# Kernel tuning notes

Measured on AMD Instinct MI355X. Metric: run time of the kernel, lower is better.

Reference implementation:

```python
import jax, jax.numpy as jnp
import numpy as np

N_HEAD = 16
CHUNK_SIZE = 64
TOP_B = 8
LOCAL_WINDOW = 256


def _l2_normalize(x, eps=1e-12):
    # matches torch F.normalize(dim=-1): x / max(||x||, eps)
    n = jnp.sqrt(jnp.sum(x * x, axis=-1, keepdims=True))
    return x / jnp.maximum(n, eps)


def setup_inputs() -> dict:
    key = jax.random.key(0)
    ks = jax.random.split(key, 9)
    B, T, C = 2, 2048, 1024
    s = lambda fan_in: 1.0 / np.sqrt(fan_in)
    return {
        "x": jax.random.normal(ks[0], (B, T, C), jnp.float32),
        "Wqkv": jax.random.normal(ks[1], (C, 3 * C), jnp.float32) * s(C),
        "bqkv": jax.random.normal(ks[2], (3 * C,), jnp.float32) * 0.02,
        "Wproj": jax.random.normal(ks[3], (C, C), jnp.float32) * s(C),
        "bproj": jax.random.normal(ks[4], (C,), jnp.float32) * 0.02,
        "Wrouter": jax.random.normal(ks[5], (C, 32), jnp.float32) * s(C),
        "brouter": jax.random.normal(ks[6], (32,), jnp.float32) * 0.02,
        "Wq_rt": jax.random.normal(ks[7], (C, 32), jnp.float32) * s(C),
        "bq_rt": jax.random.normal(ks[8], (32,), jnp.float32) * 0.02,
    }


def reference(x, Wqkv, bqkv, Wproj, bproj, Wrouter, brouter, Wq_rt, bq_rt):
    B, T, C = x.shape
    H = N_HEAD
    D = C // H

    # --- qkv projection ---
    qkv = x @ Wqkv + bqkv                       # [B,T,3C]
    q, k, v = jnp.split(qkv, 3, axis=-1)
    q = q.reshape(B, T, H, D).transpose(0, 2, 1, 3)  # [B,H,T,D]
    k = k.reshape(B, T, H, D).transpose(0, 2, 1, 3)
    v = v.reshape(B, T, H, D).transpose(0, 2, 1, 3)

    # --- routing (T > local_window + chunk_size) ---
    num_chunks = T // CHUNK_SIZE                 # T divisible -> no padding, mask all-True
    chunk_means = x.reshape(B, num_chunks, CHUNK_SIZE, C).mean(axis=2)  # [B,N,C]
    routing_embeds = chunk_means @ Wrouter + brouter                     # [B,N,32]
    q_rt = _l2_normalize(x @ Wq_rt + bq_rt)                              # [B,T,32]
    re_n = _l2_normalize(routing_embeds)
    routing_scores = jnp.einsum('btd,bnd->btn', q_rt, re_n)              # [B,T,N]
    _, chunk_indices = jax.lax.top_k(routing_scores, TOP_B)              # [B,T,top_b]

    # --- dense causal attention (forward path uses is_causal SDPA) ---
    scale = 1.0 / jnp.sqrt(jnp.asarray(D, x.dtype))
    scores = jnp.einsum('bhqd,bhkd->bhqk', q, k) * scale                 # [B,H,T,T]
    causal = jnp.tril(jnp.ones((T, T), dtype=bool))
    scores = jnp.where(causal[None, None], scores, -jnp.inf)
    attn = jax.nn.softmax(scores, axis=-1)
    y = jnp.einsum('bhqk,bhkd->bhqd', attn, v)                           # [B,H,T,D]
    y = y.transpose(0, 2, 1, 3).reshape(B, T, C)
    y = y @ Wproj + bproj

    return y, chunk_indices, routing_scores, routing_embeds
```

## Files before the change

kernel.cpp:

```cpp
#include <hip/hip_runtime.h>
#include <hip/hip_bf16.h>
#include <math.h>

#define B_   2
#define T_   2048
#define C_   1024
#define H_   16
#define D_   64
#define NCH  32
#define RD   32
#define TOPB 8

typedef __attribute__((ext_vector_type(8))) short bf16x8;
typedef __attribute__((ext_vector_type(4))) float f32x4;

static __device__ __forceinline__ unsigned short f2b(float f) {
    return __bfloat16_as_ushort(__float2bfloat16(f));
}
static __device__ __forceinline__ float b2f(unsigned short u) {
    union { unsigned u32; float f; } c; c.u32 = ((unsigned)u) << 16; return c.f;
}

#define SCALE2 0.18033688f

__global__ __launch_bounds__(256) void prep_fused(
    const float* __restrict__ x, unsigned short* __restrict__ xb,
    const float* __restrict__ Wqkv, unsigned short* __restrict__ Wqt,
    const float* __restrict__ Wproj, unsigned short* __restrict__ Wpt,
    const float* __restrict__ Wq_rt, const float* __restrict__ bq_rt,
    float* __restrict__ qrt, float* __restrict__ cm)
{
    __shared__ float smem[64 * 65];
    const int bid = blockIdx.x;
    const int tid = threadIdx.x;

    if (bid < 1024) {
        const float* W; unsigned short* Wt; int N, local;
        if (bid < 768) { W = Wqkv;  Wt = Wqt; N = 3072; local = bid; }
        else           { W = Wproj; Wt = Wpt; N = 1024; local = bid - 768; }
        const int nblk = N >> 6;
        const int n0 = (local % nblk) * 64, k0 = (local / nblk) * 64;
        float (*t)[65] = (float(*)[65])smem;
#pragma unroll
        for (int i = 0; i < 4; i++) {
            const int f = tid + i * 256;
            const int r = f >> 4, c4 = (f & 15) * 4;
            float4 v = *(const float4*)&W[(size_t)(k0 + r) * N + n0 + c4];
            t[r][c4 + 0] = v.x; t[r][c4 + 1] = v.y;
            t[r][c4 + 2] = v.z; t[r][c4 + 3] = v.w;
        }
        __syncthreads();
#pragma unroll
        for (int i = 0; i < 2; i++) {
            const int s = tid + i * 256;
            const int rn = s >> 3, ck8 = (s & 7) * 8;
            bf16x8 o;
#pragma unroll
            for (int j = 0; j < 8; j++) o[j] = (short)f2b(t[ck8 + j][rn]);
            *(bf16x8*)&Wt[(size_t)(n0 + rn) * 1024 + k0 + ck8] = o;
        }
    } else if (bid < 2048) {
        float (*part)[4][32] = (float(*)[4][32])smem;
        const int r0 = (bid - 1024) * 4;
        const int g = tid >> 5;
        const int n = tid & 31;
        const float* w  = Wq_rt + (size_t)(g * 128) * RD + n;
        const float* a0 = x + (size_t)(r0 + 0) * C_ + g * 128;
        const float* a1 = x + (size_t)(r0 + 1) * C_ + g * 128;
        const float* a2 = x + (size_t)(r0 + 2) * C_ + g * 128;
        const float* a3 = x + (size_t)(r0 + 3) * C_ + g * 128;
        float acc0 = 0.f, acc1 = 0.f, acc2 = 0.f, acc3 = 0.f;
#pragma unroll 8
        for (int i = 0; i < 128; i += 4) {
            const float w0 = w[(i + 0) * RD];
            const float w1 = w[(i + 1) * RD];
            const float w2 = w[(i + 2) * RD];
            const float w3 = w[(i + 3) * RD];
            float4 x0 = *(const float4*)&a0[i];
            float4 x1 = *(const float4*)&a1[i];
            float4 x2 = *(const float4*)&a2[i];
            float4 x3 = *(const float4*)&a3[i];
            acc0 += x0.x * w0; acc0 += x0.y * w1; acc0 += x0.z * w2; acc0 += x0.w * w3;
            acc1 += x1.x * w0; acc1 += x1.y * w1; acc1 += x1.z * w2; acc1 += x1.w * w3;
            acc2 += x2.x * w0; acc2 += x2.y * w1; acc2 += x2.z * w2; acc2 += x2.w * w3;
            acc3 += x3.x * w0; acc3 += x3.y * w1; acc3 += x3.z * w2; acc3 += x3.w * w3;
        }
        part[g][0][n] = acc0;
        part[g][1][n] = acc1;
        part[g][2][n] = acc2;
        part[g][3][n] = acc3;
        __syncthreads();
        if (g < 4) {
            float s = part[0][g][n];
#pragma unroll
            for (int gg = 1; gg < 8; gg++) s += part[gg][g][n];
            s += bq_rt[n];
            float ss = s * s;
#pragma unroll
            for (int off = 16; off >= 1; off >>= 1) ss += __shfl_xor(ss, off, 32);
            qrt[(size_t)(r0 + g) * RD + n] = s / fmaxf(sqrtf(ss), 1e-12f);
        }
    } else {
        const int local = bid - 2048;
        const int bc = local & 63;
        const int b = bc >> 5, n = bc & 31;
        const int c = (local >> 6) * 256 + tid;
        const size_t rowbase = ((size_t)b * T_ + n * 64) * C_ + c;
        float s = 0.f;
        for (int i = 0; i < 64; i++) {
            const float v = x[rowbase + (size_t)i * C_];
            s += v;
            xb[rowbase + (size_t)i * C_] = f2b(v);
        }
        cm[(size_t)bc * C_ + c] = s * (1.0f / 64.0f);
    }
}

__global__ void embeds_kernel(const float* __restrict__ cm, const float* __restrict__ W,
                              const float* __restrict__ bias,
                              float* __restrict__ emb_out, float* __restrict__ ren)
{
    const int row  = blockIdx.x * 8 + (threadIdx.x >> 5);
    const int lane = threadIdx.x & 31;
    if (row >= B_ * NCH) return;
    const float* a = cm + (size_t)row * C_;
    float acc = 0.f;
    for (int k = 0; k < C_; k += 4) {
        float4 a4 = *(const float4*)&a[k];
        acc += a4.x * W[(k + 0) * RD + lane];
        acc += a4.y * W[(k + 1) * RD + lane];
        acc += a4.z * W[(k + 2) * RD + lane];
        acc += a4.w * W[(k + 3) * RD + lane];
    }
    acc += bias[lane];
    emb_out[(size_t)row * RD + lane] = acc;
    float ss = acc * acc;
#pragma unroll
    for (int off = 16; off >= 1; off >>= 1) ss += __shfl_xor(ss, off, 32);
    ren[(size_t)row * RD + lane] = acc / fmaxf(sqrtf(ss), 1e-12f);
}

__global__ __launch_bounds__(512, 4) void gemm_qkv_128x256(
    const unsigned short* __restrict__ A, const unsigned short* __restrict__ Bt,
    const float* __restrict__ bias,
    unsigned short* __restrict__ qp, unsigned short* __restrict__ kp,
    unsigned short* __restrict__ vp, int M, int N, int K)
{
    __shared__ unsigned short lds[3][12288];

    const int tid  = threadIdx.x;
    const int wid  = tid >> 6;
    const int lane = tid & 63;
    const int lr = lane & 15, lg = lane >> 4;
    const int wm = wid >> 2;
    const int wn = wid & 3;

    const int bid = blockIdx.x;
    const int swz = (bid & 7) * 48 + (bid >> 3);
    const int m0 = (swz & 31) << 7;
    const int n0 = (swz >> 5) << 8;

    const int srow = tid >> 2;
    const int sswz = (((srow & 3) ^ ((srow >> 2) & 3)) << 4);
    const int skel = (((tid & 3) << 4) ^ sswz) >> 1;
    const unsigned short* gA  = A  + (size_t)(m0 + srow) * K + skel;
    const unsigned short* gB0 = Bt + (size_t)(n0 + srow) * K + skel;
    const unsigned short* gB1 = Bt + (size_t)(n0 + srow + 128) * K + skel;
    const int lb = wid * 512;

#define QSTAGE(sl, kofs)                                                          \
    __builtin_amdgcn_global_load_lds(                                             \
        (const __attribute__((address_space(1))) int*)(gA + (kofs)),              \
        (__attribute__((address_space(3))) int*)&lds[sl][lb], 16, 0, 0);          \
    __builtin_amdgcn_global_load_lds(                                             \
        (const __attribute__((address_space(1))) int*)(gB0 + (kofs)),             \
        (__attribute__((address_space(3))) int*)&lds[sl][4096 + lb], 16, 0, 0);   \
    __builtin_amdgcn_global_load_lds(                                             \
        (const __attribute__((address_space(1))) int*)(gB1 + (kofs)),             \
        (__attribute__((address_space(3))) int*)&lds[sl][8192 + lb], 16, 0, 0);

    const int rswz = (((lr & 3) ^ ((lr >> 2) & 3)) << 4);
    const int acol = (((lg << 4) ^ rswz) >> 1);

    f32x4 acc[4][4];
#pragma unroll
    for (int i = 0; i < 4; i++)
#pragma unroll
        for (int j = 0; j < 4; j++) acc[i][j] = (f32x4){0.f, 0.f, 0.f, 0.f};

    const int nt = K >> 5;

    QSTAGE(0, 0)
    QSTAGE(1, 32)
    asm volatile("s_waitcnt vmcnt(3)" ::: "memory");
    __builtin_amdgcn_s_barrier();

    int cur = 0;
    for (int t = 0; t < nt; ++t) {
        int s2 = cur + 2; if (s2 >= 3) s2 -= 3;
        if (t + 2 < nt) { QSTAGE(s2, (t + 2) << 5) }

        const unsigned short* sA = &lds[cur][0];
        const unsigned short* sB = &lds[cur][4096];

        bf16x8 af[4], bfr[4];
#pragma unroll
        for (int mi = 0; mi < 4; mi++)
            af[mi] = *(const bf16x8*)&sA[(wm * 64 + mi * 16 + lr) * 32 + acol];
#pragma unroll
        for (int ni = 0; ni < 4; ni++)
            bfr[ni] = *(const bf16x8*)&sB[(wn * 64 + ni * 16 + lr) * 32 + acol];

        __builtin_amdgcn_s_setprio(1);
#pragma unroll
        for (int mi = 0; mi < 4; mi++)
#pragma unroll
            for (int ni = 0; ni < 4; ni++)
                acc[mi][ni] = __builtin_amdgcn_mfma_f32_16x16x32_bf16(
                    af[mi], bfr[ni], acc[mi][ni], 0, 0, 0);
        __builtin_amdgcn_s_setprio(0);

        if (t + 1 < nt) {
            if (t + 2 < nt) { asm volatile("s_waitcnt vmcnt(3)" ::: "memory"); }
            else            { asm volatile("s_waitcnt vmcnt(0)" ::: "memory"); }
            __builtin_amdgcn_s_barrier();
        }
        cur += 1; if (cur == 3) cur = 0;
    }
#undef QSTAGE

#pragma unroll
    for (int ni = 0; ni < 4; ni++) {
        const int col = n0 + wn * 64 + ni * 16 + lr;
        const float bv = bias[col];
        const int which = col >> 10;
        const int c  = col & 1023;
        const int hh = c >> 6;
        const int dd = c & 63;
        unsigned short* dst = (which == 0) ? qp : (which == 1) ? kp : vp;
        const float postmul = (which == 0) ? SCALE2 : 1.0f;
#pragma unroll
        for (int mi = 0; mi < 4; mi++) {
#pragma unroll
            for (int r = 0; r < 4; r++) {
                const int row = m0 + wm * 64 + mi * 16 + lg * 4 + r;
                const int bb = row >> 11, tt = row & 2047;
                dst[(((size_t)bb * H_ + hh) * T_ + tt) * D_ + dd] =
                    f2b((acc[mi][ni][r] + bv) * postmul);
            }
        }
    }
}

__global__ __launch_bounds__(256, 1) void gemm_proj_128(
    const unsigned short* __restrict__ A, const unsigned short* __restrict__ Bt,
    const float* __restrict__ bias, float* __restrict__ out, int M, int N, int K)
{
    __shared__ unsigned short lds[3][2][4096];

    const int tid  = threadIdx.x;
    const int lane = tid & 63;
    const int wave = tid >> 6;
    const int lr = lane & 15, lg = lane >> 4;
    const int wm = wave >> 1, wn = wave & 1;
    const int n0 = blockIdx.x * 128, m0 = blockIdx.y * 128;

    const int srow = tid >> 2;
    const int sswz = (((srow & 3) ^ ((srow >> 2) & 3)) << 4);
    const int skel = (((tid & 3) << 4) ^ sswz) >> 1;
    const unsigned short* gA0 = A  + (size_t)(m0 + srow) * K + skel;
    const unsigned short* gA1 = A  + (size_t)(m0 + srow + 64) * K + skel;
    const unsigned short* gB0 = Bt + (size_t)(n0 + srow) * K + skel;
    const unsigned short* gB1 = Bt + (size_t)(n0 + srow + 64) * K + skel;
    const int ldb = (tid & 0xC0) * 8;

#define PSTAGE(sl, kofs)                                                          \
    __builtin_amdgcn_global_load_lds(                                             \
        (const __attribute__((address_space(1))) int*)(gA0 + (kofs)),             \
        (__attribute__((address_space(3))) int*)&lds[sl][0][ldb], 16, 0, 0);      \
    __builtin_amdgcn_global_load_lds(                                             \
        (const __attribute__((address_space(1))) int*)(gA1 + (kofs)),             \
        (__attribute__((address_space(3))) int*)&lds[sl][0][2048 + ldb], 16, 0, 0); \
    __builtin_amdgcn_global_load_lds(                                             \
        (const __attribute__((address_space(1))) int*)(gB0 + (kofs)),             \
        (__attribute__((address_space(3))) int*)&lds[sl][1][ldb], 16, 0, 0);      \
    __builtin_amdgcn_global_load_lds(                                             \
        (const __attribute__((address_space(1))) int*)(gB1 + (kofs)),             \
        (__attribute__((address_space(3))) int*)&lds[sl][1][2048 + ldb], 16, 0, 0);

    const int rswz = (((lr & 3) ^ ((lr >> 2) & 3)) << 4);
    const int acol = (((lg << 4) ^ rswz) >> 1);

    f32x4 acc[4][4];
#pragma unroll
    for (int i = 0; i < 4; i++)
#pragma unroll
        for (int j = 0; j < 4; j++) acc[i][j] = (f32x4){0.f, 0.f, 0.f, 0.f};

    const int nt = K >> 5;

    PSTAGE(0, 0)
    PSTAGE(1, 32)
    asm volatile("s_waitcnt vmcnt(4)" ::: "memory");
    __builtin_amdgcn_s_barrier();

    int cur = 0;
    for (int t = 0; t < nt; ++t) {
        int s2 = cur + 2; if (s2 >= 3) s2 -= 3;
        if (t + 2 < nt) { PSTAGE(s2, (t + 2) << 5) }

        const unsigned short* sA = &lds[cur][0][0];
        const unsigned short* sB = &lds[cur][1][0];

        bf16x8 af[4], bfr[4];
#pragma unroll
        for (int mi = 0; mi < 4; mi++)
            af[mi] = *(const bf16x8*)&sA[(wm * 64 + mi * 16 + lr) * 32 + acol];
#pragma unroll
        for (int ni = 0; ni < 4; ni++)
            bfr[ni] = *(const bf16x8*)&sB[(wn * 64 + ni * 16 + lr) * 32 + acol];

        __builtin_amdgcn_s_setprio(1);
#pragma unroll
        for (int mi = 0; mi < 4; mi++)
#pragma unroll
            for (int ni = 0; ni < 4; ni++)
                acc[mi][ni] = __builtin_amdgcn_mfma_f32_16x16x32_bf16(
                    af[mi], bfr[ni], acc[mi][ni], 0, 0, 0);
        __builtin_amdgcn_s_setprio(0);

        if (t + 1 < nt) {
            if (t + 2 < nt) { asm volatile("s_waitcnt vmcnt(4)" ::: "memory"); }
            else            { asm volatile("s_waitcnt vmcnt(0)" ::: "memory"); }
            __builtin_amdgcn_s_barrier();
        }
        cur += 1; if (cur == 3) cur = 0;
    }
#undef PSTAGE

#pragma unroll
    for (int ni = 0; ni < 4; ni++) {
        const int col = n0 + wn * 64 + ni * 16 + lr;
        const float bv = bias[col];
#pragma unroll
        for (int mi = 0; mi < 4; mi++) {
#pragma unroll
            for (int r = 0; r < 4; r++) {
                const int row = m0 + wm * 64 + mi * 16 + lg * 4 + r;
                out[(size_t)row * N + col] = acc[mi][ni][r] + bv;
            }
        }
    }
}

__global__ void scores_topk(const float* __restrict__ qrt, const float* __restrict__ ren,
                            float* __restrict__ sc_out, float* __restrict__ idx_out)
{
    const int row = blockIdx.x * 64 + threadIdx.x;
    if (row >= B_ * T_) return;
    const int b = row / T_;
    float q[RD];
#pragma unroll
    for (int i = 0; i < RD; i++) q[i] = qrt[(size_t)row * RD + i];
    const float* rb = ren + (size_t)b * NCH * RD;
    float s[NCH];
#pragma unroll 4
    for (int n = 0; n < NCH; n++) {
        float acc = 0.f;
#pragma unroll
        for (int i = 0; i < RD; i++) acc += q[i] * rb[n * RD + i];
        s[n] = acc;
        sc_out[(size_t)row * NCH + n] = acc;
    }
    unsigned mask = 0;
    for (int t = 0; t < TOPB; t++) {
        float best = -INFINITY;
        int bi = 0;
#pragma unroll
        for (int n = 0; n < NCH; n++) {
            const bool ok = !((mask >> n) & 1u) && (s[n] > best);
            if (ok) { best = s[n]; bi = n; }
        }
        mask |= (1u << bi);
        idx_out[(size_t)row * TOPB + t] = (float)bi;
    }
}

#define SW(row, idx) ((idx) ^ (((row) & 7) << 3))

__global__ __launch_bounds__(256) void attn_mfma(
    const unsigned short* __restrict__ qg, const unsigned short* __restrict__ kg,
    const unsigned short* __restrict__ vg,
    unsigned short* __restrict__ Op0, unsigned short* __restrict__ Op1,
    float2* __restrict__ mlbuf)
{
    const int bid  = blockIdx.x;
    const int xcd  = bid & 7;
    const int h    = xcd + 8 * ((bid >> 3) & 1);
    const int b    = (bid >> 4) & 1;
    const int rest = bid >> 5;
    const int half = rest & 1;
    const int i    = rest >> 1;
    const int qt   = 31 - i;

    const int tid  = threadIdx.x;
    const int wave = tid >> 6;
    const int lane = tid & 63;
    const int lg = lane >> 4;
    const int lr = lane & 15;

    const int bh = b * H_ + h;

    const int ntt = qt + 1;
    const int nh0 = (ntt + 1) >> 1;
    const int kts = half ? nh0 : 0;
    const int kte = half ? ntt : nh0;

    float m_run = -INFINITY, l_run = 0.f;

    if (kts >= kte) {
        if (lg == 0 && wave < 4) {
            const int trow = qt * 64 + wave * 16 + lr;
            mlbuf[(size_t)half * (B_ * H_ * T_) + (size_t)bh * T_ + trow] =
                make_float2(-INFINITY, 0.f);
        }
        return;
    }

    __shared__ short Ks[2][64 * 64];
    __shared__ short Vt[2][64 * 64];

    const size_t base = ((size_t)bh * T_) * D_;

    bf16x8 qf0, qf1;
    {
        const short* qp = (const short*)qg + base + (size_t)(qt * 64 + wave * 16 + lr) * D_;
        qf0 = *(const bf16x8*)&qp[lg * 8];
        qf1 = *(const bf16x8*)&qp[32 + lg * 8];
    }

    const int srr = tid >> 2;
    const int sc0 = (tid & 3) * 16;
    const int vrp = tid & 31;
    const int vcg = tid >> 5;
    const int kv0   = 2 * vrp;
    const int vslot = ((kv0 >> 5) << 5) + (((kv0 >> 2) & 3) << 3) +
                      (((kv0 >> 4) & 1) << 2) + (kv0 & 3);

    const int kst0 = SW(srr, srr * 64 + sc0);
    const int kst1 = SW(srr, srr * 64 + sc0 + 8);
    const int rsw = (lr & 7) << 3;

    bf16x8 kreg0, kreg1, vreg0, vreg1;

    f32x4 oacc[4];
#pragma unroll
    for (int r = 0; r < 4; r++) oacc[r] = (f32x4){0.f, 0.f, 0.f, 0.f};
    const int qrow_g = qt * 64 + wave * 16 + lr;

#define VPACK(buf)                                                              \
    {                                                                           \
        const unsigned* v0d = (const unsigned*)&vreg0;                          \
        const unsigned* v1d = (const unsigned*)&vreg1;                          \
        _Pragma("unroll")                                                       \
        for (int jj = 0; jj < 8; jj++) {                                        \
            const unsigned sel = (jj & 1) ? 0x07060302u : 0x05040100u;          \
            const unsigned dw = __builtin_amdgcn_perm(v1d[jj >> 1], v0d[jj >> 1], sel); \
            *(unsigned*)&Vt[buf][SW(jj, (vcg * 8 + jj) * 64 + vslot)] = dw;     \
        }                                                                       \
    }

    const short* kpn = (const short*)kg + base + (size_t)(kts * 64 + srr) * D_ + sc0;
    const short* vpn = (const short*)vg + base + (size_t)(kts * 64 + kv0) * D_ + vcg * 8;

    kreg0 = *(const bf16x8*)kpn;
    kreg1 = *(const bf16x8*)(kpn + 8);
    vreg0 = *(const bf16x8*)vpn;
    vreg1 = *(const bf16x8*)(vpn + D_);
    kpn += 4096; vpn += 4096;

    *(bf16x8*)&Ks[0][kst0] = kreg0;
    *(bf16x8*)&Ks[0][kst1] = kreg1;
    VPACK(0)

    if (kts + 1 < kte) {
        kreg0 = *(const bf16x8*)kpn;
        kreg1 = *(const bf16x8*)(kpn + 8);
        vreg0 = *(const bf16x8*)vpn;
        vreg1 = *(const bf16x8*)(vpn + D_);
        kpn += 4096; vpn += 4096;
    }
    __syncthreads();

    for (int kt = kts; kt < kte; ++kt) {
        const int cur = (kt - kts) & 1;

        if (kt + 1 < kte) {
            *(bf16x8*)&Ks[cur ^ 1][kst0] = kreg0;
            *(bf16x8*)&Ks[cur ^ 1][kst1] = kreg1;
            VPACK(cur ^ 1)
        }
        if (kt + 2 < kte) {
            kreg0 = *(const bf16x8*)kpn;
            kreg1 = *(const bf16x8*)(kpn + 8);
            vreg0 = *(const bf16x8*)vpn;
            vreg1 = *(const bf16x8*)(vpn + D_);
            kpn += 4096; vpn += 4096;
        }

        f32x4 s[4];
        __builtin_amdgcn_s_setprio(1);
#pragma unroll
        for (int cb = 0; cb < 4; cb++) {
            const int row = cb * 16 + lr;
            bf16x8 kf0 = *(const bf16x8*)&Ks[cur][(row * 64 + lg * 8) ^ rsw];
            bf16x8 kf1 = *(const bf16x8*)&Ks[cur][(row * 64 + 32 + lg * 8) ^ rsw];
            f32x4 acc = (f32x4){0.f, 0.f, 0.f, 0.f};
            acc = __builtin_amdgcn_mfma_f32_16x16x32_bf16(kf0, qf0, acc, 0, 0, 0);
            acc = __builtin_amdgcn_mfma_f32_16x16x32_bf16(kf1, qf1, acc, 0, 0, 0);
            s[cb] = acc;
        }
        __builtin_amdgcn_s_setprio(0);

        if (kt == qt) {
#pragma unroll
            for (int cb = 0; cb < 4; cb++)
#pragma unroll
                for (int r = 0; r < 4; r++)
                    if (kt * 64 + cb * 16 + lg * 4 + r > qrow_g) s[cb][r] = -INFINITY;
        }

        float rm;
        {
            const float t0 = fmaxf(fmaxf(s[0][0], s[0][1]), fmaxf(s[0][2], s[0][3]));
            const float t1 = fmaxf(fmaxf(s[1][0], s[1][1]), fmaxf(s[1][2], s[1][3]));
            const float t2 = fmaxf(fmaxf(s[2][0], s[2][1]), fmaxf(s[2][2], s[2][3]));
            const float t3 = fmaxf(fmaxf(s[3][0], s[3][1]), fmaxf(s[3][2], s[3][3]));
            rm = fmaxf(fmaxf(t0, t1), fmaxf(t2, t3));
        }
        rm = fmaxf(rm, __shfl_xor(rm, 16));
        rm = fmaxf(rm, __shfl_xor(rm, 32));

        if (!__all(rm <= m_run + 8.0f)) {
            const float mnew = fmaxf(m_run, rm);
            const float fsc  = exp2f(m_run - mnew);
            m_run = mnew;
            l_run *= fsc;
            float fr[4];
#pragma unroll
            for (int r = 0; r < 4; r++) fr[r] = __shfl(fsc, lg * 4 + r);
#pragma unroll
            for (int db = 0; db < 4; db++)
#pragma unroll
                for (int r = 0; r < 4; r++) oacc[db][r] *= fr[r];
        }

        float p[4][4];
#pragma unroll
        for (int cb = 0; cb < 4; cb++)
#pragma unroll
            for (int r = 0; r < 4; r++)
                p[cb][r] = exp2f(s[cb][r] - m_run);
        float rs;
        {
            const float t0 = (p[0][0] + p[0][1]) + (p[0][2] + p[0][3]);
            const float t1 = (p[1][0] + p[1][1]) + (p[1][2] + p[1][3]);
            const float t2 = (p[2][0] + p[2][1]) + (p[2][2] + p[2][3]);
            const float t3 = (p[3][0] + p[3][1]) + (p[3][2] + p[3][3]);
            rs = (t0 + t1) + (t2 + t3);
        }
        rs += __shfl_xor(rs, 16);
        rs += __shfl_xor(rs, 32);
        l_run += rs;

        bf16x8 pf0, pf1;
#pragma unroll
        for (int r = 0; r < 4; r++) {
            pf0[r]     = (short)f2b(p[0][r]);
            pf0[4 + r] = (short)f2b(p[1][r]);
            pf1[r]     = (short)f2b(p[2][r]);
            pf1[4 + r] = (short)f2b(p[3][r]);
        }

        __builtin_amdgcn_s_setprio(1);
#pragma unroll
        for (int db = 0; db < 4; db++) {
            const int row = db * 16 + lr;
            bf16x8 vf0 = *(const bf16x8*)&Vt[cur][(row * 64 + lg * 8) ^ rsw];
            bf16x8 vf1 = *(const bf16x8*)&Vt[cur][(row * 64 + 32 + lg * 8) ^ rsw];
            oacc[db] = __builtin_amdgcn_mfma_f32_16x16x32_bf16(pf0, vf0, oacc[db], 0, 0, 0);
            oacc[db] = __builtin_amdgcn_mfma_f32_16x16x32_bf16(pf1, vf1, oacc[db], 0, 0, 0);
        }
        __builtin_amdgcn_s_setprio(0);

        __syncthreads();
    }
#undef VPACK

    unsigned short* Op = half ? Op1 : Op0;
#pragma unroll
    for (int r = 0; r < 4; r++) {
        const int trow = qt * 64 + wave * 16 + lg * 4 + r;
        unsigned short* op = Op + ((size_t)bh * T_ + trow) * D_;
#pragma unroll
        for (int db = 0; db < 4; db++)
            op[db * 16 + lr] = f2b(oacc[db][r]);
    }
    if (lg == 0) {
        const int trow = qt * 64 + wave * 16 + lr;
        mlbuf[(size_t)half * (B_ * H_ * T_) + (size_t)bh * T_ + trow] =
            make_float2(m_run, l_run);
    }
}

__global__ __launch_bounds__(256) void combine_kernel(
    const unsigned short* __restrict__ Op0, const unsigned short* __restrict__ Op1,
    const float2* __restrict__ mlbuf, unsigned short* __restrict__ y)
{
    const int ro = blockIdx.x * 16 + (threadIdx.x >> 4);
    const int d0 = (threadIdx.x & 15) * 4;

    const float2 ml0 = mlbuf[ro];
    const float2 ml1 = mlbuf[B_ * H_ * T_ + ro];
    const float m  = fmaxf(ml0.x, ml1.x);
    const float w0 = exp2f(ml0.x - m);
    const float w1 = exp2f(ml1.x - m);
    const float inv = 1.0f / (ml0.y * w0 + ml1.y * w1);

    const size_t off = (size_t)ro * D_ + d0;
    const ushort4 o0 = *(const ushort4*)&Op0[off];
    const ushort4 o1 = *(const ushort4*)&Op1[off];

    ushort4 res;
    res.x = f2b((b2f(o0.x) * w0 + b2f(o1.x) * w1) * inv);
    res.y = f2b((b2f(o0.y) * w0 + b2f(o1.y) * w1) * inv);
    res.z = f2b((b2f(o0.z) * w0 + b2f(o1.z) * w1) * inv);
    res.w = f2b((b2f(o0.w) * w0 + b2f(o1.w) * w1) * inv);

    const int bh = ro >> 11, t = ro & 2047;
    const int b = bh >> 4, h = bh & 15;
    *(ushort4*)&y[((size_t)(b * T_ + t) * C_) + h * D_ + d0] = res;
}

extern "C" void kernel_launch(void* const* d_in, const int* in_sizes, int n_in,
                              void* d_out, int out_size, void* d_ws, size_t ws_size,
                              hipStream_t stream)
{
    const float* x       = (const float*)d_in[0];
    const float* Wqkv    = (const float*)d_in[1];
    const float* bqkv    = (const float*)d_in[2];
    const float* Wproj   = (const float*)d_in[3];
    const float* bproj   = (const float*)d_in[4];
    const float* Wrouter = (const float*)d_in[5];
    const float* brouter = (const float*)d_in[6];
    const float* Wq_rt   = (const float*)d_in[7];
    const float* bq_rt   = (const float*)d_in[8];

    float* out = (float*)d_out;
    char*  ws  = (char*)d_ws;

    const size_t MT  = (size_t)B_ * T_;
    const size_t QKV = MT * C_;

    unsigned short* xb   = (unsigned short*)ws;
    unsigned short* Wqt  = xb  + QKV;
    unsigned short* Wpt  = Wqt + (size_t)3 * C_ * C_;
    unsigned short* q    = Wpt + (size_t)C_ * C_;
    unsigned short* k    = q + QKV;
    unsigned short* v    = k + QKV;
    unsigned short* yab  = v + QKV;
    float* cm   = (float*)(yab + QKV);
    float* qrt  = cm  + (size_t)B_ * NCH * C_;
    float* ren  = qrt + MT * RD;
    float2* mlbuf = (float2*)(ren + (size_t)B_ * NCH * RD);
    unsigned short* Op1 = (unsigned short*)(mlbuf + 2 * B_ * H_ * T_);
    unsigned short* Op0 = xb;

    float* y_out   = out;
    float* idx_out = out + QKV;
    float* sc_out  = idx_out + MT * TOPB;
    float* emb_out = sc_out + MT * NCH;

    prep_fused<<<2304, 256, 0, stream>>>(x, xb, Wqkv, Wqt, Wproj, Wpt,
                                         Wq_rt, bq_rt, qrt, cm);

    gemm_qkv_128x256<<<dim3(384), 512, 0, stream>>>(
        xb, Wqt, bqkv, q, k, v, (int)MT, 3 * C_, C_);

    embeds_kernel<<<8, 256, 0, stream>>>(cm, Wrouter, brouter, emb_out, ren);
    scores_topk<<<(int)(MT / 64), 64, 0, stream>>>(qrt, ren, sc_out, idx_out);

    attn_mfma<<<dim3(2048), 256, 0, stream>>>(q, k, v, Op0, Op1, mlbuf);
    combine_kernel<<<dim3(4096), 256, 0, stream>>>(Op0, Op1, mlbuf, yab);

    gemm_proj_128<<<dim3(C_ / 128, MT / 128), 256, 0, stream>>>(
        yab, Wpt, bproj, y_out, (int)MT, C_, C_);
}
```

Baseline: 175.7 us.

## Single-buffer K/V LDS tiles in attention and raise occupancy hint

Replaces the double-buffered K and V shared-memory tiles with single buffers, which halves LDS use per block. The next tile is now written from registers to LDS between two barriers after the PV MFMAs. Global loads are still prefetched into registers one tile ahead. It also adds a launch-bounds minimum of 8 blocks per CU so more blocks can be resident. The trade-off is an extra barrier per iteration and no overlap between LDS stores and MFMA work, and the occupancy hint may limit registers per thread.

```diff
diff --git a/kernel.cpp b/kernel.cpp
--- a/kernel.cpp
+++ b/kernel.cpp
@@ -388,7 +388,7 @@
 
 #define SW(row, idx) ((idx) ^ (((row) & 7) << 3))
 
-__global__ __launch_bounds__(256) void attn_mfma(
+__global__ __launch_bounds__(256, 8) void attn_mfma(
     const unsigned short* __restrict__ qg, const unsigned short* __restrict__ kg,
     const unsigned short* __restrict__ vg,
     unsigned short* __restrict__ Op0, unsigned short* __restrict__ Op1,
@@ -427,8 +427,8 @@
         return;
     }
 
-    __shared__ short Ks[2][64 * 64];
-    __shared__ short Vt[2][64 * 64];
+    __shared__ short Ks[64 * 64];
+    __shared__ short Vt[64 * 64];
 
     const size_t base = ((size_t)bh * T_) * D_;
 
@@ -458,7 +458,7 @@
     for (int r = 0; r < 4; r++) oacc[r] = (f32x4){0.f, 0.f, 0.f, 0.f};
     const int qrow_g = qt * 64 + wave * 16 + lr;
 
-#define VPACK(buf)                                                              \
+#define VPACK()                                                                 \
     {                                                                           \
         const unsigned* v0d = (const unsigned*)&vreg0;                          \
         const unsigned* v1d = (const unsigned*)&vreg1;                          \
@@ -466,7 +466,7 @@
         for (int jj = 0; jj < 8; jj++) {                                        \
             const unsigned sel = (jj & 1) ? 0x07060302u : 0x05040100u;          \
             const unsigned dw = __builtin_amdgcn_perm(v1d[jj >> 1], v0d[jj >> 1], sel); \
-            *(unsigned*)&Vt[buf][SW(jj, (vcg * 8 + jj) * 64 + vslot)] = dw;     \
+            *(unsigned*)&Vt[SW(jj, (vcg * 8 + jj) * 64 + vslot)] = dw;          \
         }                                                                       \
     }
 
@@ -479,9 +479,9 @@
     vreg1 = *(const bf16x8*)(vpn + D_);
     kpn += 4096; vpn += 4096;
 
-    *(bf16x8*)&Ks[0][kst0] = kreg0;
-    *(bf16x8*)&Ks[0][kst1] = kreg1;
-    VPACK(0)
+    *(bf16x8*)&Ks[kst0] = kreg0;
+    *(bf16x8*)&Ks[kst1] = kreg1;
+    VPACK()
 
     if (kts + 1 < kte) {
         kreg0 = *(const bf16x8*)kpn;
@@ -493,28 +493,13 @@
     __syncthreads();
 
     for (int kt = kts; kt < kte; ++kt) {
-        const int cur = (kt - kts) & 1;
-
-        if (kt + 1 < kte) {
-            *(bf16x8*)&Ks[cur ^ 1][kst0] = kreg0;
-            *(bf16x8*)&Ks[cur ^ 1][kst1] = kreg1;
-            VPACK(cur ^ 1)
-        }
-        if (kt + 2 < kte) {
-            kreg0 = *(const bf16x8*)kpn;
-            kreg1 = *(const bf16x8*)(kpn + 8);
-            vreg0 = *(const bf16x8*)vpn;
-            vreg1 = *(const bf16x8*)(vpn + D_);
-            kpn += 4096; vpn += 4096;
-        }
-
         f32x4 s[4];
         __builtin_amdgcn_s_setprio(1);
 #pragma unroll
         for (int cb = 0; cb < 4; cb++) {
             const int row = cb * 16 + lr;
-            bf16x8 kf0 = *(const bf16x8*)&Ks[cur][(row * 64 + lg * 8) ^ rsw];
-            bf16x8 kf1 = *(const bf16x8*)&Ks[cur][(row * 64 + 32 + lg * 8) ^ rsw];
+            bf16x8 kf0 = *(const bf16x8*)&Ks[(row * 64 + lg * 8) ^ rsw];
+            bf16x8 kf1 = *(const bf16x8*)&Ks[(row * 64 + 32 + lg * 8) ^ rsw];
             f32x4 acc = (f32x4){0.f, 0.f, 0.f, 0.f};
             acc = __builtin_amdgcn_mfma_f32_16x16x32_bf16(kf0, qf0, acc, 0, 0, 0);
             acc = __builtin_amdgcn_mfma_f32_16x16x32_bf16(kf1, qf1, acc, 0, 0, 0);
@@ -586,14 +571,27 @@
 #pragma unroll
         for (int db = 0; db < 4; db++) {
             const int row = db * 16 + lr;
-            bf16x8 vf0 = *(const bf16x8*)&Vt[cur][(row * 64 + lg * 8) ^ rsw];
-            bf16x8 vf1 = *(const bf16x8*)&Vt[cur][(row * 64 + 32 + lg * 8) ^ rsw];
+            bf16x8 vf0 = *(const bf16x8*)&Vt[(row * 64 + lg * 8) ^ rsw];
+            bf16x8 vf1 = *(const bf16x8*)&Vt[(row * 64 + 32 + lg * 8) ^ rsw];
             oacc[db] = __builtin_amdgcn_mfma_f32_16x16x32_bf16(pf0, vf0, oacc[db], 0, 0, 0);
             oacc[db] = __builtin_amdgcn_mfma_f32_16x16x32_bf16(pf1, vf1, oacc[db], 0, 0, 0);
         }
         __builtin_amdgcn_s_setprio(0);
 
-        __syncthreads();
+        if (kt + 1 < kte) {
+            __syncthreads();
+            *(bf16x8*)&Ks[kst0] = kreg0;
+            *(bf16x8*)&Ks[kst1] = kreg1;
+            VPACK()
+            if (kt + 2 < kte) {
+                kreg0 = *(const bf16x8*)kpn;
+                kreg1 = *(const bf16x8*)(kpn + 8);
+                vreg0 = *(const bf16x8*)vpn;
+                vreg1 = *(const bf16x8*)(vpn + D_);
+                kpn += 4096; vpn += 4096;
+            }
+            __syncthreads();
+        }
     }
 #undef VPACK
 
```

Result: slower. 292.7 us (+66.6%).
